# Performance work log

Hardware: AMD Instinct MI355X
Metric: run time of the kernel (lower is better)

The kernel has to match this reference:

```python
import jax, jax.numpy as jnp
import numpy as np

Z, N, K, W = 131072, 64, 64, 32


def setup_inputs() -> dict:
    key = jax.random.key(0)
    k1, k2, k3 = jax.random.split(key, 3)
    features = jax.random.normal(k1, (Z, N), dtype=jnp.float32)
    # dense realization of the CG-derived mixing tensor 'wkij'
    mixing_matrix = jax.random.normal(k2, (W, K, N, N), dtype=jnp.float32) * 0.05
    weight = jax.random.normal(k3, (W,), dtype=jnp.float32)
    return {"features": features, "mixing_matrix": mixing_matrix, "weight": weight}


def reference(features, mixing_matrix, weight):
    # torch: einsum('w,wkij,zi,zj->zk', weight, mixing_matrix, features, features)
    # Contract the small path axis w first -> [K, N, N] (cheap, tiny output),
    # then the bilinear square over z. einsum chooses a GEMM-style path; the
    # [Z, N, N] outer-product side is the memory-bound part.
    M = jnp.einsum('w,wkij->kij', weight, mixing_matrix)  # [K, N, N]
    out = jnp.einsum('kij,zi,zj->zk', M, features, features)  # [Z, K]
    return out
```

## Files before the change

### kernel.cpp

```cpp
#include <hip/hip_runtime.h>
#include <stdint.h>

typedef __attribute__((ext_vector_type(8))) _Float16 half8;
typedef __attribute__((ext_vector_type(2))) _Float16 h2;
typedef __attribute__((ext_vector_type(4))) float f32x4;

#define NCHUNK 32

static __device__ __forceinline__ unsigned short f2h(float f) {
  return __builtin_bit_cast(unsigned short, (_Float16)f);
}
static __device__ __forceinline__ float h2f_(unsigned short s) {
  return (float)__builtin_bit_cast(_Float16, s);
}
static __device__ __forceinline__ void gload16(const void* g, void* l) {
  __builtin_amdgcn_global_load_lds((const __attribute__((address_space(1))) void*)g,
                                   (__attribute__((address_space(3))) void*)l, 16, 0, 0);
}

__global__ __launch_bounds__(256) void prep_kernel(const float* __restrict__ mix,
                                                   const float* __restrict__ wgt,
                                                   unsigned short* __restrict__ Bp) {
  __shared__ float4 red[256];
  const int tid = threadIdx.x;
  const int ws  = tid >> 6;
  const int tt  = tid & 63;
  const int t4  = blockIdx.x * 64 + tt;
  const float4* m4 = (const float4*)mix;
  float ax = 0.f, ay = 0.f, az = 0.f, aw = 0.f;
#pragma unroll
  for (int wi = 0; wi < 8; ++wi) {
    const int w = ws * 8 + wi;
    const float s = wgt[w];
    const float4 v = m4[w * 65536 + t4];
    ax += s * v.x; ay += s * v.y; az += s * v.z; aw += s * v.w;
  }
  red[tid] = (float4){ax, ay, az, aw};
  __syncthreads();
  if (tid < 64) {
    const float4 a = red[tid], b = red[tid + 64], c = red[tid + 128], d = red[tid + 192];
    ushort4 r;
    r.x = f2h(a.x + b.x + c.x + d.x);
    r.y = f2h(a.y + b.y + c.y + d.y);
    r.z = f2h(a.z + b.z + c.z + d.z);
    r.w = f2h(a.w + b.w + c.w + d.w);
    ((ushort4*)Bp)[blockIdx.x * 64 + tid] = r;
  }
}

__global__ __launch_bounds__(256) void symm_kernel(unsigned short* __restrict__ Bp) {
  unsigned short* B = Bp + (size_t)blockIdx.x * 4096;
  for (int t = threadIdx.x; t < 4096; t += 256) {
    const int i = t >> 6, j = t & 63;
    if (i < j) {
      const int tt = (j << 6) | i;
      const float a = h2f_(B[t]);
      const float b = h2f_(B[tt]);
      B[t]  = f2h(a + b);
      B[tt] = 0;
    }
  }
}

__global__ __launch_bounds__(512, 4) void gemm_kernel(const float* __restrict__ X,
                                                      const unsigned short* __restrict__ Bp,
                                                      float* __restrict__ out) {
  __shared__ unsigned short ldsB[2][64 * 128];
  __shared__ unsigned short sH[2][2][128];

  const int tid  = threadIdx.x;
  const int lane = tid & 63;
  const int wv   = tid >> 6;
  const int wz   = wv >> 1;
  const int wk   = wv & 1;
  const int m    = lane & 15;
  const int q    = lane >> 4;
  const int zblk = blockIdx.x * 128;

  auto stageB = [&](int ct, int bf) {
#pragma unroll
    for (int it = 0; it < 2; ++it) {
      const int seg = wv * 2 + it;
      const int row = seg * 4 + (lane >> 4);
      const int u   = (lane & 15) ^ (row & 15);
      gload16(Bp + (size_t)row * 4096 + ct * 128 + u * 8,
              &ldsB[bf][seg * 512]);
    }
  };

  stageB(0, 0);
  if (tid < 128) {
    const float2 xp = *(const float2*)(X + (size_t)(zblk + tid) * 64);
    const int d  = (tid >> 5) * 16 + (tid & 15);
    const int hf = (tid >> 4) & 1;
    sH[0][0][d * 2 + hf] = f2h(xp.x);
    sH[0][1][d * 2 + hf] = f2h(xp.y);
  }

  h2 jh[2][8];
  {
    const float4* X4g = (const float4*)X;
#pragma unroll
    for (int f = 0; f < 2; ++f) {
      const int zg = zblk + wz * 32 + f * 16 + m;
#pragma unroll
      for (int h = 0; h < 2; ++h) {
        const float4 a = X4g[zg * 16 + h * 8 + q * 2];
        const float4 b = X4g[zg * 16 + h * 8 + q * 2 + 1];
        jh[f][h * 4 + 0] = h2{(_Float16)a.x, (_Float16)a.y};
        jh[f][h * 4 + 1] = h2{(_Float16)a.z, (_Float16)a.w};
        jh[f][h * 4 + 2] = h2{(_Float16)b.x, (_Float16)b.y};
        jh[f][h * 4 + 3] = h2{(_Float16)b.z, (_Float16)b.w};
      }
    }
  }

  f32x4 acc[2][2];
#pragma unroll
  for (int f = 0; f < 2; ++f)
#pragma unroll
    for (int g = 0; g < 2; ++g) acc[f][g] = f32x4{0.f, 0.f, 0.f, 0.f};

  __syncthreads();

  auto chunk_body = [&](int c, bool full) {
    const int cn = (c + 1) & (NCHUNK - 1);
    stageB(cn, (c + 1) & 1);
    float2 spre = {0.f, 0.f};
    if (tid < 128)
      spre = *(const float2*)(X + (size_t)(zblk + tid) * 64 + cn * 2);

    const unsigned short* Bl = &ldsB[c & 1][0];
#pragma unroll
    for (int il = 0; il < 2; ++il) {
      const unsigned sv = *(const unsigned*)(&sH[c & 1][il][(wz * 16 + m) * 2]);
      h2 s2f[2];
      s2f[0] = __builtin_bit_cast(h2, __builtin_amdgcn_perm(sv, sv, 0x01000100u));
      s2f[1] = __builtin_bit_cast(h2, __builtin_amdgcn_perm(sv, sv, 0x03020302u));
      auto hblk = [&](int h) {
        const int u = ((il << 3) + (h << 2) + q) ^ m;
        const unsigned short* bb = Bl + (wk * 32 + m) * 128 + u * 8;
        const half8 b0 = *(const half8*)(const void*)(bb);
        const half8 b1 = *(const half8*)(const void*)(bb + 16 * 128);
#pragma unroll
        for (int f = 0; f < 2; ++f) {
          union { unsigned u[4]; half8 v; } A;
#pragma unroll
          for (int e = 0; e < 4; ++e) {
            const h2 pr = s2f[f] * jh[f][h * 4 + e];
            A.u[e] = __builtin_bit_cast(unsigned, pr);
          }
          acc[f][0] = __builtin_amdgcn_mfma_f32_16x16x32_f16(A.v, b0, acc[f][0], 0, 0, 0);
          acc[f][1] = __builtin_amdgcn_mfma_f32_16x16x32_f16(A.v, b1, acc[f][1], 0, 0, 0);
        }
      };
      if (full) hblk(0);
      hblk(1);
    }

    if (tid < 128) {
      const int d  = (tid >> 5) * 16 + (tid & 15);
      const int hf = (tid >> 4) & 1;
      sH[(c + 1) & 1][0][d * 2 + hf] = f2h(spre.x);
      sH[(c + 1) & 1][1][d * 2 + hf] = f2h(spre.y);
    }
    __syncthreads();
  };

  for (int c = 0; c < 16; ++c)      chunk_body(c, true);
  for (int c = 16; c < NCHUNK; ++c) chunk_body(c, false);

#pragma unroll
  for (int f = 0; f < 2; ++f) {
    const int zr = zblk + wz * 32 + f * 16 + q * 4;
#pragma unroll
    for (int g = 0; g < 2; ++g)
#pragma unroll
      for (int r = 0; r < 4; ++r)
        out[(size_t)(zr + r) * 64 + wk * 32 + g * 16 + m] = acc[f][g][r];
  }
}

extern "C" void kernel_launch(void* const* d_in, const int* in_sizes, int n_in,
                              void* d_out, int out_size, void* d_ws, size_t ws_size,
                              hipStream_t stream) {
  const float* X   = (const float*)d_in[0];
  const float* mix = (const float*)d_in[1];
  const float* wgt = (const float*)d_in[2];
  float* out = (float*)d_out;
  unsigned short* Bp = (unsigned short*)d_ws;

  prep_kernel<<<1024, 256, 0, stream>>>(mix, wgt, Bp);
  symm_kernel<<<64, 256, 0, stream>>>(Bp);
  gemm_kernel<<<1024, 512, 0, stream>>>(X, Bp, out);
}
```

Baseline: 164.8 us.

## Double per-block Z tile and triple-buffer B staging with explicit waitcnt

Each block now covers 256 rows of Z instead of 128, with four 16-row fragments per wave, so each staged B chunk in LDS is reused across twice as many rows and the grid is halved. B staging moves to a three-deep ring that prefetches two chunks ahead, and __syncthreads is replaced by explicit vmcnt/lgkmcnt waits plus s_barrier so loads can stay in flight across iterations. The costs are more accumulator and jh registers, which can lower occupancy under launch_bounds(512,4), and fewer blocks to spread across CUs.

```diff
diff --git a/kernel.cpp b/kernel.cpp
--- a/kernel.cpp
+++ b/kernel.cpp
@@ -65,8 +65,8 @@
 __global__ __launch_bounds__(512, 4) void gemm_kernel(const float* __restrict__ X,
                                                       const unsigned short* __restrict__ Bp,
                                                       float* __restrict__ out) {
-  __shared__ unsigned short ldsB[2][64 * 128];
-  __shared__ unsigned short sH[2][2][128];
+  __shared__ unsigned short ldsB[3][64 * 128];
+  __shared__ unsigned short sH[2][2][256];
 
   const int tid  = threadIdx.x;
   const int lane = tid & 63;
@@ -75,7 +75,7 @@
   const int wk   = wv & 1;
   const int m    = lane & 15;
   const int q    = lane >> 4;
-  const int zblk = blockIdx.x * 128;
+  const int zblk = blockIdx.x * 256;
 
   auto stageB = [&](int ct, int bf) {
 #pragma unroll
@@ -88,21 +88,29 @@
     }
   };
 
+  auto publishS = [&](int bf, float2 xp) {
+    if (tid < 256) {
+      const int d  = (tid >> 6) * 32 + (tid & 15) * 2 + ((tid >> 5) & 1);
+      const int hf = (tid >> 4) & 1;
+      sH[bf][0][d * 2 + hf] = f2h(xp.x);
+      sH[bf][1][d * 2 + hf] = f2h(xp.y);
+    }
+  };
+
   stageB(0, 0);
-  if (tid < 128) {
-    const float2 xp = *(const float2*)(X + (size_t)(zblk + tid) * 64);
-    const int d  = (tid >> 5) * 16 + (tid & 15);
-    const int hf = (tid >> 4) & 1;
-    sH[0][0][d * 2 + hf] = f2h(xp.x);
-    sH[0][1][d * 2 + hf] = f2h(xp.y);
-  }
-
-  h2 jh[2][8];
+  stageB(1, 1);
+  {
+    float2 xp0 = {0.f, 0.f};
+    if (tid < 256) xp0 = *(const float2*)(X + (size_t)(zblk + tid) * 64);
+    publishS(0, xp0);
+  }
+
+  h2 jh[4][8];
   {
     const float4* X4g = (const float4*)X;
 #pragma unroll
-    for (int f = 0; f < 2; ++f) {
-      const int zg = zblk + wz * 32 + f * 16 + m;
+    for (int f = 0; f < 4; ++f) {
+      const int zg = zblk + wz * 64 + f * 16 + m;
 #pragma unroll
       for (int h = 0; h < 2; ++h) {
         const float4 a = X4g[zg * 16 + h * 8 + q * 2];
@@ -115,35 +123,40 @@
     }
   }
 
-  f32x4 acc[2][2];
-#pragma unroll
-  for (int f = 0; f < 2; ++f)
+  f32x4 acc[4][2];
+#pragma unroll
+  for (int f = 0; f < 4; ++f)
 #pragma unroll
     for (int g = 0; g < 2; ++g) acc[f][g] = f32x4{0.f, 0.f, 0.f, 0.f};
 
   __syncthreads();
 
-  auto chunk_body = [&](int c, bool full) {
+  int bufc = 0;
+  for (int c = 0; c < NCHUNK; ++c) {
     const int cn = (c + 1) & (NCHUNK - 1);
-    stageB(cn, (c + 1) & 1);
     float2 spre = {0.f, 0.f};
-    if (tid < 128)
+    if (tid < 256)
       spre = *(const float2*)(X + (size_t)(zblk + tid) * 64 + cn * 2);
-
-    const unsigned short* Bl = &ldsB[c & 1][0];
+    int bs = bufc + 2; if (bs >= 3) bs -= 3;
+    stageB((c + 2) & (NCHUNK - 1), bs);
+
+    const unsigned short* Bl = &ldsB[bufc][0];
+    const bool full = (c < 16);
 #pragma unroll
     for (int il = 0; il < 2; ++il) {
-      const unsigned sv = *(const unsigned*)(&sH[c & 1][il][(wz * 16 + m) * 2]);
-      h2 s2f[2];
-      s2f[0] = __builtin_bit_cast(h2, __builtin_amdgcn_perm(sv, sv, 0x01000100u));
-      s2f[1] = __builtin_bit_cast(h2, __builtin_amdgcn_perm(sv, sv, 0x03020302u));
+      const uint2 sv = *(const uint2*)(&sH[c & 1][il][wz * 64 + m * 4]);
+      h2 s2f[4];
+      s2f[0] = __builtin_bit_cast(h2, __builtin_amdgcn_perm(sv.x, sv.x, 0x01000100u));
+      s2f[1] = __builtin_bit_cast(h2, __builtin_amdgcn_perm(sv.x, sv.x, 0x03020302u));
+      s2f[2] = __builtin_bit_cast(h2, __builtin_amdgcn_perm(sv.y, sv.y, 0x01000100u));
+      s2f[3] = __builtin_bit_cast(h2, __builtin_amdgcn_perm(sv.y, sv.y, 0x03020302u));
       auto hblk = [&](int h) {
         const int u = ((il << 3) + (h << 2) + q) ^ m;
         const unsigned short* bb = Bl + (wk * 32 + m) * 128 + u * 8;
         const half8 b0 = *(const half8*)(const void*)(bb);
         const half8 b1 = *(const half8*)(const void*)(bb + 16 * 128);
 #pragma unroll
-        for (int f = 0; f < 2; ++f) {
+        for (int f = 0; f < 4; ++f) {
           union { unsigned u[4]; half8 v; } A;
 #pragma unroll
           for (int e = 0; e < 4; ++e) {
@@ -158,21 +171,17 @@
       hblk(1);
     }
 
-    if (tid < 128) {
-      const int d  = (tid >> 5) * 16 + (tid & 15);
-      const int hf = (tid >> 4) & 1;
-      sH[(c + 1) & 1][0][d * 2 + hf] = f2h(spre.x);
-      sH[(c + 1) & 1][1][d * 2 + hf] = f2h(spre.y);
-    }
-    __syncthreads();
-  };
-
-  for (int c = 0; c < 16; ++c)      chunk_body(c, true);
-  for (int c = 16; c < NCHUNK; ++c) chunk_body(c, false);
-
-#pragma unroll
-  for (int f = 0; f < 2; ++f) {
-    const int zr = zblk + wz * 32 + f * 16 + q * 4;
+    publishS(cn & 1, spre);
+    asm volatile("s_waitcnt vmcnt(2)" ::: "memory");
+    asm volatile("s_waitcnt lgkmcnt(0)" ::: "memory");
+    __builtin_amdgcn_s_barrier();
+    __builtin_amdgcn_sched_barrier(0);
+    bufc = (bufc + 1 == 3) ? 0 : bufc + 1;
+  }
+
+#pragma unroll
+  for (int f = 0; f < 4; ++f) {
+    const int zr = zblk + wz * 64 + f * 16 + q * 4;
 #pragma unroll
     for (int g = 0; g < 2; ++g)
 #pragma unroll
@@ -192,5 +201,5 @@
 
   prep_kernel<<<1024, 256, 0, stream>>>(mix, wgt, Bp);
   symm_kernel<<<64, 256, 0, stream>>>(Bp);
-  gemm_kernel<<<1024, 512, 0, stream>>>(X, Bp, out);
-}
+  gemm_kernel<<<512, 512, 0, stream>>>(X, Bp, out);
+}
```

Result: faster. 161.1 us (-2.3%).
